# Performance work log

Measured on AMD Instinct MI355X. Metric: run time of the kernel, lower is better.

## Reference

```python
import jax, jax.numpy as jnp
import numpy as np

B, DIM, H, W = 32, 512, 48, 24


def conv1x1(x, w, b):
    # x: [B,C,H,W], w: [O,C], b: [O]  (torch Conv2d 1x1 weight squeezed)
    return jnp.einsum('bchw,oc->bohw', x, w) + b[None, :, None, None]


def setup_inputs() -> dict:
    key = jax.random.key(0)
    ks = jax.random.split(key, 14)
    s = 0.02
    inp = {
        'x': jax.random.normal(ks[0], (B, DIM, H, W), jnp.float32),
        'x_h': jax.random.normal(ks[1], (B, DIM, H, W), jnp.float32),
        'Wg': jax.random.normal(ks[2], (DIM, DIM), jnp.float32) * s,
        'bg': jax.random.normal(ks[3], (DIM,), jnp.float32) * s,
        'Wt': jax.random.normal(ks[4], (DIM, DIM), jnp.float32) * s,
        'bt': jax.random.normal(ks[5], (DIM,), jnp.float32) * s,
        'Wp': jax.random.normal(ks[6], (DIM, DIM), jnp.float32) * s,
        'bp': jax.random.normal(ks[7], (DIM,), jnp.float32) * s,
        'Ww': jax.random.normal(ks[8], (DIM, DIM), jnp.float32) * s,
        'bw': jax.random.normal(ks[9], (DIM,), jnp.float32) * s,
        'gamma': jax.random.normal(ks[10], (DIM,), jnp.float32) * 0.1,
        'beta': jax.random.normal(ks[11], (DIM,), jnp.float32) * 0.1,
        'run_mean': jax.random.normal(ks[12], (DIM,), jnp.float32) * 0.1,
        'run_var': jax.random.uniform(ks[13], (DIM,), jnp.float32, 0.5, 1.5),
    }
    return inp


def reference(x, x_h, Wg, bg, Wt, bt, Wp, bp, Ww, bw, gamma, beta, run_mean, run_var):
    Bsz, dim = x.shape[0], Wg.shape[0]
    g_x = conv1x1(x_h, Wg, bg).reshape(Bsz, dim, -1)      # [B,dim,N]
    theta_x = conv1x1(x, Wt, bt).reshape(Bsz, dim, -1)    # [B,dim,N]
    phi_x = conv1x1(x_h, Wp, bp).reshape(Bsz, dim, -1)    # [B,dim,N]
    # energy[b,i,j] = sum_n theta[b,i,n] * phi[b,j,n]  -> channel attention [B,dim,dim]
    energy = jnp.einsum('bin,bjn->bij', theta_x, phi_x)
    attention = energy / dim  # energy.size(-1) == dim
    y = jnp.einsum('bij,bjn->bin', attention, g_x).reshape(Bsz, dim, *x_h.shape[2:])
    W_y = conv1x1(y, Ww, bw)
    # BatchNorm2d in eval mode
    inv = gamma / jnp.sqrt(run_var + 1e-5)
    W_y = (W_y - run_mean[None, :, None, None]) * inv[None, :, None, None] + beta[None, :, None, None]
    return W_y + x
```

## Files before the change

kernel.cpp:

```cpp
#include <hip/hip_runtime.h>
#include <stdint.h>

typedef short short8 __attribute__((ext_vector_type(8)));
typedef float f32x4 __attribute__((ext_vector_type(4)));
typedef unsigned short u16;
typedef unsigned int u32;

struct alignas(8) U16x4 { u16 x, y, z, w; };

__device__ __forceinline__ u16 f2bf(float f) {
  u32 u = __float_as_uint(f);
  u += 0x7fffu + ((u >> 16) & 1u);
  return (u16)(u >> 16);
}
__device__ __forceinline__ float bf2f(u16 v) {
  return __uint_as_float(((u32)v) << 16);
}

__device__ __forceinline__ void gld_lds16(const u16* g, u16* l) {
  __builtin_amdgcn_global_load_lds((const __attribute__((address_space(1))) u32*)g,
                                   (__attribute__((address_space(3))) u32*)l,
                                   16, 0, 0);
}

__device__ __forceinline__ void mfma16x16x32(f32x4& c, short8 a, short8 b) {
  asm("v_mfma_f32_16x16x32_bf16 %0, %1, %2, %0" : "+v"(c) : "v"(a), "v"(b));
}

__device__ __forceinline__ float wave_red(float v) {
  for (int off = 32; off; off >>= 1) v += __shfl_down(v, off);
  return v;
}

template<int EPI>
__global__ void __launch_bounds__(512, 2) gemm_abt(
                         const u16* __restrict__ A, int64_t Abs,
                         const u16* __restrict__ Bt, int64_t Bbs,
                         void* __restrict__ Cptr, int64_t Cbs,
                         int M, int N, int K,
                         const float* __restrict__ v1,
                         const float* __restrict__ v2,
                         const float* __restrict__ v3,
                         const float* __restrict__ v4,
                         const u16* __restrict__ xres) {
  constexpr int BM = 256, BN = 128, BK = 32;
  extern __shared__ u16 lds[];
  u16* ldsA = lds;
  u16* ldsB = lds + 4 * (BM * BK);

  int bx, by, b;
  if (gridDim.z == 1) {
    const int nbx = N >> 7;
    const int bpb = nbx * (M >> 8);
    const int id = blockIdx.x;
    const int xcd = id & 7, rest = id >> 3;
    b = xcd + 8 * (rest / bpb);
    const int wi = rest % bpb;
    by = wi / nbx; bx = wi % nbx;
  } else {
    bx = blockIdx.x; by = blockIdx.y; b = blockIdx.z;
  }

  const u16* Ab = A + (int64_t)b * Abs;
  const u16* Bb = Bt + (int64_t)b * Bbs;
  const int brow = by * BM, bcol = bx * BN;
  const int tid = threadIdx.x, lane = tid & 63, w = tid >> 6;
  const int wr = w >> 1, wc = w & 1;

  f32x4 acc[4][4] = {};

  const int sr = tid >> 2;
  const int scs = ((tid & 3) ^ (sr & 3)) * 8;
  const int lo = sr * BK + (tid & 3) * 8;
  const u16* gA = Ab + (int64_t)(brow + sr) * K + scs;
  const u16* gB = Bb + (int64_t)(bcol + sr) * K + scs;

  const int la16 = lane & 15;
  const int kg = (lane >> 4) * 8;
  const int kc = kg ^ ((la16 & 3) * 8);
  const int nt = K / BK;

#define STAGE(buf, k0)                                              \
  do {                                                              \
    u16* la_ = ldsA + (buf) * (BM * BK) + lo;                       \
    u16* lb_ = ldsB + (buf) * (BN * BK) + lo;                       \
    gld_lds16(gA + (k0), la_);                                      \
    gld_lds16(gA + (int64_t)128 * K + (k0), la_ + 128 * BK);        \
    gld_lds16(gB + (k0), lb_);                                      \
  } while (0)

  STAGE(0, 0);
  STAGE(1, BK);
  STAGE(2, 2 * BK);

  for (int t = 0; t < nt; ++t) {
    __builtin_amdgcn_s_barrier();
    if (t + 3 < nt) {
      STAGE((t + 3) & 3, (t + 3) * BK);
      asm volatile("s_waitcnt vmcnt(9)" ::: "memory");
    } else {
      const int rem = nt - 1 - t;
      if (rem == 2)      asm volatile("s_waitcnt vmcnt(6)" ::: "memory");
      else if (rem == 1) asm volatile("s_waitcnt vmcnt(3)" ::: "memory");
      else               asm volatile("s_waitcnt vmcnt(0)" ::: "memory");
    }
    __builtin_amdgcn_s_barrier();
    __builtin_amdgcn_sched_barrier(0);
    const u16* as = ldsA + (t & 3) * (BM * BK);
    const u16* bs = ldsB + (t & 3) * (BN * BK);
    short8 af[4], bf[4];
#pragma unroll
    for (int m = 0; m < 4; ++m)
      af[m] = *(const short8*)&as[(wr * 64 + m * 16 + la16) * BK + kc];
#pragma unroll
    for (int n = 0; n < 4; ++n)
      bf[n] = *(const short8*)&bs[(wc * 64 + n * 16 + la16) * BK + kc];
    __builtin_amdgcn_s_setprio(1);
#pragma unroll
    for (int m = 0; m < 4; ++m)
#pragma unroll
      for (int n = 0; n < 4; ++n)
        mfma16x16x32(acc[m][n], af[m], bf[n]);
    __builtin_amdgcn_s_setprio(0);
  }
#undef STAGE
  asm volatile("s_nop 7\n\ts_nop 7");

  const int r0 = brow + wr * 64 + (lane >> 4) * 4;
  const int c0 = bcol + wc * 64 + la16;
  const int64_t b512 = (int64_t)b * 512;

  if (EPI == 4) {
    float* Cb = (float*)Cptr + (int64_t)b * Cbs;
    const u16* xb = xres + (int64_t)b * Cbs;
#pragma unroll
    for (int m = 0; m < 4; ++m) {
#pragma unroll
      for (int r = 0; r < 4; ++r) {
        const int row = r0 + m * 16 + r;
        const float scl = v1[row], shf = v2[b512 + row];
#pragma unroll
        for (int n = 0; n < 4; ++n) {
          const int col = c0 + n * 16;
          Cb[(int64_t)row * N + col] =
              acc[m][n][r] * scl + shf + bf2f(xb[(int64_t)row * N + col]);
        }
      }
    }
  } else {
    u16* Cb = (u16*)Cptr + (int64_t)b * Cbs;
#pragma unroll
    for (int m = 0; m < 4; ++m) {
#pragma unroll
      for (int r = 0; r < 4; ++r) {
        const int row = r0 + m * 16 + r;
        float a1 = 0.f, a3 = 0.f;
        if (EPI == 6) { a1 = v1[b512 + row]; a3 = v3[row]; }
#pragma unroll
        for (int n = 0; n < 4; ++n) {
          const int col = c0 + n * 16;
          float v = acc[m][n][r];
          if (EPI == 6) v += a1 * v2[col] + a3 * v4[b512 + col];
          Cb[(int64_t)row * N + col] = f2bf(v);
        }
      }
    }
  }
}

__global__ void cvt_rows(const float* __restrict__ x, const float* __restrict__ xh,
                         u16* __restrict__ xB, u16* __restrict__ xhB,
                         float* __restrict__ rx, float* __restrict__ rxh) {
  const bool h = blockIdx.y != 0;
  const float* in = h ? xh : x;
  u16* out = h ? xhB : xB;
  float* rs = h ? rxh : rx;
  const int t = threadIdx.x;
  const int64_t row = (int64_t)blockIdx.x * 8 + (t >> 5);
  const int l = t & 31;
  const float4* ib = (const float4*)(in + row * 1152);
  U16x4* ob = (U16x4*)(out + row * 1152);
  float s = 0.f;
#pragma unroll
  for (int i = 0; i < 9; ++i) {
    const float4 v = ib[l + i * 32];
    s += v.x + v.y + v.z + v.w;
    U16x4 o = {f2bf(v.x), f2bf(v.y), f2bf(v.z), f2bf(v.w)};
    ob[l + i * 32] = o;
  }
#pragma unroll
  for (int off = 16; off; off >>= 1) s += __shfl_down(s, off, 32);
  if (l == 0) rs[row] = s;
}

__global__ void transpose_bf_reg(const u16* __restrict__ in, u16* __restrict__ out) {
  const int b = blockIdx.z;
  const u16* ib = in + (int64_t)b * 589824;
  u16* ob = out + (int64_t)b * 589824;
  const int t = threadIdx.x;
  const int c0 = blockIdx.y * 128 + (t & 15) * 8;
  const int n0 = blockIdx.x * 128 + (t >> 4) * 8;
  short8 r[8];
#pragma unroll
  for (int k = 0; k < 8; ++k)
    r[k] = *(const short8*)&ib[(int64_t)(c0 + k) * 1152 + n0];
#pragma unroll
  for (int i = 0; i < 8; ++i) {
    short8 wv;
#pragma unroll
    for (int k = 0; k < 8; ++k) wv[k] = r[k][i];
    *(short8*)&ob[(int64_t)(n0 + i) * 512 + c0] = wv;
  }
}

__global__ void transpose_cvt4(const float* __restrict__ s0, const float* __restrict__ s1,
                               const float* __restrict__ s2, const float* __restrict__ s3,
                               u16* __restrict__ d0, u16* __restrict__ d1,
                               u16* __restrict__ d2, u16* __restrict__ d3) {
  const int z = blockIdx.z;
  const float* in = z == 0 ? s0 : z == 1 ? s1 : z == 2 ? s2 : s3;
  u16* out = z == 0 ? d0 : z == 1 ? d1 : z == 2 ? d2 : d3;
  __shared__ float t[32][33];
  const int n0 = blockIdx.x * 32, c0 = blockIdx.y * 32;
  const int tr = threadIdx.x >> 3, tc = (threadIdx.x & 7) * 4;
  const float4 v = *(const float4*)&in[(int64_t)(c0 + tr) * 512 + n0 + tc];
  t[tr][tc] = v.x; t[tr][tc + 1] = v.y; t[tr][tc + 2] = v.z; t[tr][tc + 3] = v.w;
  __syncthreads();
  U16x4 o;
  o.x = f2bf(t[tc][tr]); o.y = f2bf(t[tc + 1][tr]);
  o.z = f2bf(t[tc + 2][tr]); o.w = f2bf(t[tc + 3][tr]);
  *(U16x4*)&out[(int64_t)(n0 + tr) * 512 + c0 + tc] = o;
}

__global__ void cvt_kernel(const float* __restrict__ in, u16* __restrict__ out, int n4) {
  const int i = blockIdx.x * 256 + threadIdx.x;
  if (i < n4) {
    const float4 v = ((const float4*)in)[i];
    U16x4 o = {f2bf(v.x), f2bf(v.y), f2bf(v.z), f2bf(v.w)};
    ((U16x4*)out)[i] = o;
  }
}

__global__ void k_small(const float* __restrict__ gamma, const float* __restrict__ beta,
                        const float* __restrict__ mean, const float* __restrict__ var,
                        const float* __restrict__ bw,
                        const float* __restrict__ bp, const float* __restrict__ bg,
                        float* __restrict__ sc2, float* __restrict__ shift0,
                        float* __restrict__ s2) {
  const int c = threadIdx.x;
  const float sc = gamma[c] * rsqrtf(var[c] + 1e-5f);
  sc2[c] = sc * (1.0f / 512.0f);
  shift0[c] = (bw[c] - mean[c]) * sc + beta[c];
  if (c < 64) {
    float p = 0;
    for (int k = c; k < 512; k += 64) p += bp[k] * bg[k];
    p = wave_red(p);
    if (c == 0) s2[0] = p;
  }
}

__global__ void k_mv1(const float* __restrict__ Wp, const float* __restrict__ Wt,
                      const float* __restrict__ Ww,
                      const u16* __restrict__ WpT, const u16* __restrict__ WgT,
                      const float* __restrict__ bg, const float* __restrict__ bt,
                      const float* __restrict__ bp,
                      const float* __restrict__ rx, const float* __restrict__ rxh,
                      float* __restrict__ sigphi, float* __restrict__ tau2,
                      float* __restrict__ h1, float* __restrict__ w1,
                      float* __restrict__ c2) {
  const int wid = blockIdx.x * 4 + (threadIdx.x >> 6);
  const int lane = threadIdx.x & 63;
  float dot = 0;
  if (wid < 16384) {
    const int b = wid >> 9, t = wid & 511;
    const float* wr = Wp + (int64_t)t * 512;
    const float* vr = rxh + b * 512;
#pragma unroll
    for (int k = 0; k < 8; ++k) dot += wr[lane + k * 64] * vr[lane + k * 64];
    dot = wave_red(dot);
    if (lane == 0) sigphi[wid] = dot;
  } else if (wid < 32768) {
    const int r = wid - 16384, b = r >> 9, t = r & 511;
    const float* wr = Wt + (int64_t)t * 512;
    const float* vr = rx + b * 512;
#pragma unroll
    for (int k = 0; k < 8; ++k) dot += wr[lane + k * 64] * vr[lane + k * 64];
    dot = wave_red(dot);
    if (lane == 0) tau2[r] = dot + 1152.0f * bt[t];
  } else if (wid < 33280) {
    const int j = wid - 32768;
    const u16* wr = WpT + (int64_t)j * 512;
#pragma unroll
    for (int k = 0; k < 8; ++k) dot += bf2f(wr[lane + k * 64]) * bg[lane + k * 64];
    dot = wave_red(dot);
    if (lane == 0) h1[j] = dot;
  } else if (wid < 33792) {
    const int c = wid - 33280;
    const float* wr = Ww + (int64_t)c * 512;
#pragma unroll
    for (int k = 0; k < 8; ++k) dot += wr[lane + k * 64] * bt[lane + k * 64];
    dot = wave_red(dot);
    if (lane == 0) w1[c] = dot;
  } else {
    const int e = wid - 33792;
    const u16* wr = WgT + (int64_t)e * 512;
#pragma unroll
    for (int k = 0; k < 8; ++k) dot += bf2f(wr[lane + k * 64]) * bp[lane + k * 64];
    dot = wave_red(dot);
    if (lane == 0) c2[e] = dot;
  }
}

__global__ void k_mv2(const u16* __restrict__ WgT, const float* __restrict__ Ww,
                      const float* __restrict__ bg,
                      const float* __restrict__ sigphi, const float* __restrict__ tau2,
                      float* __restrict__ c1, float* __restrict__ w2,
                      float* __restrict__ s1) {
  const int wid = blockIdx.x * 4 + (threadIdx.x >> 6);
  const int lane = threadIdx.x & 63;
  float dot = 0;
  if (wid < 16384) {
    const int b = wid >> 9, t = wid & 511;
    const u16* wr = WgT + (int64_t)t * 512;
    const float* vr = sigphi + b * 512;
#pragma unroll
    for (int k = 0; k < 8; ++k) dot += bf2f(wr[lane + k * 64]) * vr[lane + k * 64];
    dot = wave_red(dot);
    if (lane == 0) c1[wid] = dot;
  } else if (wid < 32768) {
    const int r = wid - 16384, b = r >> 9, t = r & 511;
    const float* wr = Ww + (int64_t)t * 512;
    const float* vr = tau2 + b * 512;
#pragma unroll
    for (int k = 0; k < 8; ++k) dot += wr[lane + k * 64] * vr[lane + k * 64];
    dot = wave_red(dot);
    if (lane == 0) w2[r] = dot;
  } else if (wid < 32800) {
    const int b = wid - 32768;
    const float* vr = sigphi + b * 512;
#pragma unroll
    for (int k = 0; k < 8; ++k) dot += vr[lane + k * 64] * bg[lane + k * 64];
    dot = wave_red(dot);
    if (lane == 0) s1[b] = dot;
  }
}

__global__ void k_shiftv(const u16* __restrict__ R, const float* __restrict__ h1,
                         const float* __restrict__ w1, const float* __restrict__ w2,
                         const float* __restrict__ s1, const float* __restrict__ s2,
                         const float* __restrict__ sc2, const float* __restrict__ shift0,
                         float* __restrict__ shiftv) {
  const int wid = blockIdx.x * 4 + (threadIdx.x >> 6);
  const int lane = threadIdx.x & 63;
  const int b = wid >> 9, c = wid & 511;
  const u16* rr = R + (int64_t)b * 262144 + (int64_t)c * 512;
  float dot = 0;
#pragma unroll
  for (int k = 0; k < 8; ++k) dot += bf2f(rr[lane + k * 64]) * h1[lane + k * 64];
  dot = wave_red(dot);
  if (lane == 0)
    shiftv[wid] = sc2[c] * (dot + s1[b] * w1[c] + s2[0] * w2[wid]) + shift0[c];
}

extern "C" void kernel_launch(void* const* d_in, const int* in_sizes, int n_in,
                              void* d_out, int out_size, void* d_ws, size_t ws_size,
                              hipStream_t stream) {
  const float* x     = (const float*)d_in[0];
  const float* x_h   = (const float*)d_in[1];
  const float* Wg    = (const float*)d_in[2];
  const float* bg    = (const float*)d_in[3];
  const float* Wt    = (const float*)d_in[4];
  const float* bt    = (const float*)d_in[5];
  const float* Wp    = (const float*)d_in[6];
  const float* bp    = (const float*)d_in[7];
  const float* Ww    = (const float*)d_in[8];
  const float* bw    = (const float*)d_in[9];
  const float* gamma = (const float*)d_in[10];
  const float* beta  = (const float*)d_in[11];
  const float* rmean = (const float*)d_in[12];
  const float* rvar  = (const float*)d_in[13];
  float* out = (float*)d_out;

  const int Bsz = 32, D = 512, N = 1152;
  const int64_t DN = (int64_t)D * N;
  const int64_t DD = (int64_t)D * D;
  const size_t LDSB = 98304;

  char* ws = (char*)d_ws;
  const size_t KB = 1024, MB = 1048576;
  u16* WtT  = (u16*)(ws + 0);
  u16* WpT  = (u16*)(ws + 512 * KB);
  u16* WwB  = (u16*)(ws + 1 * MB);
  u16* WgT  = (u16*)(ws + 1 * MB + 512 * KB);
  u16* WaB  = (u16*)(ws + 2 * MB);
  u16* WbTB = (u16*)(ws + 2 * MB + 512 * KB);
  float* rx     = (float*)(ws + 3 * MB + 512 * KB);
  float* rxh    = (float*)(ws + 3 * MB + 576 * KB);
  float* sigphi = (float*)(ws + 3 * MB + 640 * KB);
  float* tau2   = (float*)(ws + 3 * MB + 704 * KB);
  float* c1     = (float*)(ws + 3 * MB + 768 * KB);
  float* w2     = (float*)(ws + 3 * MB + 832 * KB);
  float* shiftv = (float*)(ws + 3 * MB + 896 * KB);
  float* h1     = (float*)(ws + 3 * MB + 960 * KB);
  float* w1     = (float*)(ws + 3 * MB + 962 * KB);
  float* c2     = (float*)(ws + 3 * MB + 964 * KB);
  float* sc2    = (float*)(ws + 3 * MB + 968 * KB);
  float* shift0 = (float*)(ws + 3 * MB + 970 * KB);
  float* s1     = (float*)(ws + 3 * MB + 972 * KB);
  float* s2     = (float*)(ws + 3 * MB + 974 * KB);
  u16* xB  = (u16*)(ws + 4 * MB);
  u16* xhB = (u16*)(ws + 40 * MB);
  u16* xhT = (u16*)(ws + 76 * MB);
  u16* SD1 = (u16*)(ws + 112 * MB);
  u16* SD2 = (u16*)(ws + 130 * MB);

  cvt_rows<<<dim3(Bsz * D / 8, 2), 256, 0, stream>>>(x, x_h, xB, xhB, rx, rxh);
  transpose_bf_reg<<<dim3(9, 4, Bsz), 256, 0, stream>>>(xhB, xhT);
  transpose_cvt4<<<dim3(16, 16, 3), 256, 0, stream>>>(Wt, Wp, Wg, nullptr,
                                                      WtT, WpT, WgT, nullptr);
  cvt_kernel<<<dim3(D * D / 4 / 256), 256, 0, stream>>>(Ww, WwB, D * D / 4);
  k_small<<<dim3(1), 512, 0, stream>>>(gamma, beta, rmean, rvar, bw, bp, bg,
                                       sc2, shift0, s2);
  k_mv1<<<dim3(8576), 256, 0, stream>>>(Wp, Wt, Ww, WpT, WgT, bg, bt, bp, rx, rxh,
                                        sigphi, tau2, h1, w1, c2);
  k_mv2<<<dim3(8200), 256, 0, stream>>>(WgT, Ww, bg, sigphi, tau2, c1, w2, s1);
  gemm_abt<0><<<dim3(4, 2, 2), 512, LDSB, stream>>>(
      WwB, DD, WtT, DD, WaB, DD, D, D, D, nullptr, nullptr, nullptr, nullptr, nullptr);

  gemm_abt<0><<<dim3(8 * Bsz), 512, LDSB, stream>>>(
      xhB, DN, xB, DN, SD1, DD, D, D, N, nullptr, nullptr, nullptr, nullptr, nullptr);
  gemm_abt<0><<<dim3(8 * Bsz), 512, LDSB, stream>>>(
      WaB, 0, SD1, DD, SD2, DD, D, D, D, nullptr, nullptr, nullptr, nullptr, nullptr);
  k_shiftv<<<dim3(4096), 256, 0, stream>>>(SD2, h1, w1, w2, s1, s2, sc2, shift0, shiftv);
  gemm_abt<6><<<dim3(8 * Bsz), 512, LDSB, stream>>>(
      SD2, DD, WbTB, 0, SD1, DD, D, D, D, w2, c2, w1, c1, nullptr);
  gemm_abt<4><<<dim3(18 * Bsz), 512, LDSB, stream>>>(
      SD1, DD, xhT, DN, out, DN, D, N, D, sc2, shiftv, nullptr, nullptr, xB);
}
```

Measured before the change: 213.7 us.

## Fuse x_h bf16 conversion with transpose and row-sum; use nontemporal loads/stores

Splits the combined conversion kernel into prep_x and prep_xh. prep_xh reads fp32 x_h directly, writes both the bf16 copy and the transposed bf16 copy, and produces per-tile partial row sums, so the separate transpose no longer has to re-read the bf16 buffer. The partial sums are reduced in a widened k_misc kernel that also keeps the old small-parameter work. Nontemporal loads of x and x_h and nontemporal stores of the final output are added to reduce cache pollution. The cost is an extra partial-sum buffer and a reduction step, plus a prep_xh access pattern that writes the row-major copy with strided 16-byte stores.

```diff
diff --git a/kernel.cpp b/kernel.cpp
--- a/kernel.cpp
+++ b/kernel.cpp
@@ -142,8 +142,9 @@
 #pragma unroll
         for (int n = 0; n < 4; ++n) {
           const int col = c0 + n * 16;
-          Cb[(int64_t)row * N + col] =
+          const float val =
               acc[m][n][r] * scl + shf + bf2f(xb[(int64_t)row * N + col]);
+          __builtin_nontemporal_store(val, &Cb[(int64_t)row * N + col]);
         }
       }
     }
@@ -168,48 +169,74 @@
   }
 }
 
-__global__ void cvt_rows(const float* __restrict__ x, const float* __restrict__ xh,
-                         u16* __restrict__ xB, u16* __restrict__ xhB,
-                         float* __restrict__ rx, float* __restrict__ rxh) {
-  const bool h = blockIdx.y != 0;
-  const float* in = h ? xh : x;
-  u16* out = h ? xhB : xB;
-  float* rs = h ? rxh : rx;
+__global__ void prep_x(const float* __restrict__ x, u16* __restrict__ xB,
+                       float* __restrict__ rx) {
   const int t = threadIdx.x;
-  const int64_t row = (int64_t)blockIdx.x * 8 + (t >> 5);
-  const int l = t & 31;
-  const float4* ib = (const float4*)(in + row * 1152);
-  U16x4* ob = (U16x4*)(out + row * 1152);
+  const int64_t row = (int64_t)blockIdx.x * 16 + (t >> 4);
+  const int l = t & 15;
+  const float* ib = x + row * 1152;
+  uint4* ob = (uint4*)(xB + row * 1152);
   float s = 0.f;
 #pragma unroll
   for (int i = 0; i < 9; ++i) {
-    const float4 v = ib[l + i * 32];
-    s += v.x + v.y + v.z + v.w;
-    U16x4 o = {f2bf(v.x), f2bf(v.y), f2bf(v.z), f2bf(v.w)};
-    ob[l + i * 32] = o;
-  }
-#pragma unroll
-  for (int off = 16; off; off >>= 1) s += __shfl_down(s, off, 32);
-  if (l == 0) rs[row] = s;
-}
-
-__global__ void transpose_bf_reg(const u16* __restrict__ in, u16* __restrict__ out) {
+    const int e = l * 8 + i * 128;
+    const f32x4 v0 = __builtin_nontemporal_load((const f32x4*)&ib[e]);
+    const f32x4 v1 = __builtin_nontemporal_load((const f32x4*)&ib[e + 4]);
+    s += v0[0] + v0[1] + v0[2] + v0[3] + v1[0] + v1[1] + v1[2] + v1[3];
+    u16 o[8] = {f2bf(v0[0]), f2bf(v0[1]), f2bf(v0[2]), f2bf(v0[3]),
+                f2bf(v1[0]), f2bf(v1[1]), f2bf(v1[2]), f2bf(v1[3])};
+    ob[l + i * 16] = *(uint4*)o;
+  }
+#pragma unroll
+  for (int off = 8; off; off >>= 1) s += __shfl_down(s, off, 16);
+  if (l == 0) rx[row] = s;
+}
+
+__global__ void prep_xh(const float* __restrict__ xh, u16* __restrict__ xhB,
+                        u16* __restrict__ xhT, float* __restrict__ rxh_part) {
+  __shared__ float sm[4][128];
   const int b = blockIdx.z;
-  const u16* ib = in + (int64_t)b * 589824;
-  u16* ob = out + (int64_t)b * 589824;
+  const float* src = xh + (int64_t)b * 589824;
+  u16* dB = xhB + (int64_t)b * 589824;
+  u16* dT = xhT + (int64_t)b * 589824;
   const int t = threadIdx.x;
-  const int c0 = blockIdx.y * 128 + (t & 15) * 8;
-  const int n0 = blockIdx.x * 128 + (t >> 4) * 8;
+  const int ct = t & 15, ntile = t >> 4;
+  const int c0 = blockIdx.y * 128 + ct * 8;
+  const int n0 = blockIdx.x * 128 + ntile * 8;
   short8 r[8];
-#pragma unroll
-  for (int k = 0; k < 8; ++k)
-    r[k] = *(const short8*)&ib[(int64_t)(c0 + k) * 1152 + n0];
+  float s[8];
+#pragma unroll
+  for (int k = 0; k < 8; ++k) {
+    const float* sp = &src[(int64_t)(c0 + k) * 1152 + n0];
+    const f32x4 v0 = __builtin_nontemporal_load((const f32x4*)sp);
+    const f32x4 v1 = __builtin_nontemporal_load((const f32x4*)(sp + 4));
+    s[k] = v0[0] + v0[1] + v0[2] + v0[3] + v1[0] + v1[1] + v1[2] + v1[3];
+    u16 o[8] = {f2bf(v0[0]), f2bf(v0[1]), f2bf(v0[2]), f2bf(v0[3]),
+                f2bf(v1[0]), f2bf(v1[1]), f2bf(v1[2]), f2bf(v1[3])};
+    r[k] = *(short8*)o;
+    *(uint4*)&dB[(int64_t)(c0 + k) * 1152 + n0] = *(uint4*)o;
+  }
 #pragma unroll
   for (int i = 0; i < 8; ++i) {
     short8 wv;
 #pragma unroll
     for (int k = 0; k < 8; ++k) wv[k] = r[k][i];
-    *(short8*)&ob[(int64_t)(n0 + i) * 512 + c0] = wv;
+    *(short8*)&dT[(int64_t)(n0 + i) * 512 + c0] = wv;
+  }
+#pragma unroll
+  for (int k = 0; k < 8; ++k) {
+    s[k] += __shfl_down(s[k], 32);
+    s[k] += __shfl_down(s[k], 16);
+  }
+  const int wv_ = t >> 6;
+  if ((t & 63) < 16) {
+#pragma unroll
+    for (int k = 0; k < 8; ++k) sm[wv_][ct * 8 + k] = s[k];
+  }
+  __syncthreads();
+  if (t < 128) {
+    const float v = sm[0][t] + sm[1][t] + sm[2][t] + sm[3][t];
+    rxh_part[(int64_t)blockIdx.x * 16384 + b * 512 + blockIdx.y * 128 + t] = v;
   }
 }
 
@@ -241,21 +268,31 @@
   }
 }
 
-__global__ void k_small(const float* __restrict__ gamma, const float* __restrict__ beta,
-                        const float* __restrict__ mean, const float* __restrict__ var,
-                        const float* __restrict__ bw,
-                        const float* __restrict__ bp, const float* __restrict__ bg,
-                        float* __restrict__ sc2, float* __restrict__ shift0,
-                        float* __restrict__ s2) {
-  const int c = threadIdx.x;
-  const float sc = gamma[c] * rsqrtf(var[c] + 1e-5f);
-  sc2[c] = sc * (1.0f / 512.0f);
-  shift0[c] = (bw[c] - mean[c]) * sc + beta[c];
-  if (c < 64) {
-    float p = 0;
-    for (int k = c; k < 512; k += 64) p += bp[k] * bg[k];
-    p = wave_red(p);
-    if (c == 0) s2[0] = p;
+__global__ void k_misc(const float* __restrict__ rxh_part, float* __restrict__ rxh,
+                       const float* __restrict__ gamma, const float* __restrict__ beta,
+                       const float* __restrict__ mean, const float* __restrict__ var,
+                       const float* __restrict__ bw,
+                       const float* __restrict__ bp, const float* __restrict__ bg,
+                       float* __restrict__ sc2, float* __restrict__ shift0,
+                       float* __restrict__ s2) {
+  if (blockIdx.x < 64) {
+    const int i = blockIdx.x * 256 + threadIdx.x;
+    float s = 0;
+#pragma unroll 3
+    for (int p = 0; p < 9; ++p) s += rxh_part[p * 16384 + i];
+    rxh[i] = s;
+  } else {
+    for (int c = threadIdx.x; c < 512; c += 256) {
+      const float sc = gamma[c] * rsqrtf(var[c] + 1e-5f);
+      sc2[c] = sc * (1.0f / 512.0f);
+      shift0[c] = (bw[c] - mean[c]) * sc + beta[c];
+    }
+    if (threadIdx.x < 64) {
+      float p = 0;
+      for (int k = threadIdx.x; k < 512; k += 64) p += bp[k] * bg[k];
+      p = wave_red(p);
+      if (threadIdx.x == 0) s2[0] = p;
+    }
   }
 }
 
@@ -413,14 +450,15 @@
   u16* xhT = (u16*)(ws + 76 * MB);
   u16* SD1 = (u16*)(ws + 112 * MB);
   u16* SD2 = (u16*)(ws + 130 * MB);
-
-  cvt_rows<<<dim3(Bsz * D / 8, 2), 256, 0, stream>>>(x, x_h, xB, xhB, rx, rxh);
-  transpose_bf_reg<<<dim3(9, 4, Bsz), 256, 0, stream>>>(xhB, xhT);
+  float* rxh_part = (float*)(ws + 148 * MB);
+
+  prep_x<<<dim3(Bsz * D / 16), 256, 0, stream>>>(x, xB, rx);
+  prep_xh<<<dim3(9, 4, Bsz), 256, 0, stream>>>(x_h, xhB, xhT, rxh_part);
   transpose_cvt4<<<dim3(16, 16, 3), 256, 0, stream>>>(Wt, Wp, Wg, nullptr,
                                                       WtT, WpT, WgT, nullptr);
   cvt_kernel<<<dim3(D * D / 4 / 256), 256, 0, stream>>>(Ww, WwB, D * D / 4);
-  k_small<<<dim3(1), 512, 0, stream>>>(gamma, beta, rmean, rvar, bw, bp, bg,
-                                       sc2, shift0, s2);
+  k_misc<<<dim3(65), 256, 0, stream>>>(rxh_part, rxh, gamma, beta, rmean, rvar,
+                                       bw, bp, bg, sc2, shift0, s2);
   k_mv1<<<dim3(8576), 256, 0, stream>>>(Wp, Wt, Ww, WpT, WgT, bg, bt, bp, rx, rxh,
                                         sigphi, tau2, h1, w1, c2);
   k_mv2<<<dim3(8200), 256, 0, stream>>>(WgT, Ww, bg, sigphi, tau2, c1, w2, s1);
```

Result: slower. 222.5 us (+4.1%).
